# Kernel tuning notes

Hardware: AMD Instinct MI355X
Metric: run time of the kernel (lower is better)

## Reference

```python
import jax, jax.numpy as jnp
import numpy as np
from jax import lax

B, C, T = 4, 512, 2304
H = 16
D = C // H          # 32 head dim
WIN = 19            # window_size
WOV = WIN // 2      # window_overlap = 9
W = 2 * WOV + 1     # band width = 19
EPS = 1e-5          # nn.LayerNorm default eps


def _dwconv(x, w):
    # depthwise Conv1d, kernel 3, pad 1, no bias, groups=C. x:[B,C,T], w:[C,1,3]
    return lax.conv_general_dilated(x, w, (1,), ((1, 1),),
                                    dimension_numbers=('NCH', 'OIH', 'NCH'),
                                    feature_group_count=C)


def _ln_c(x, g, b):
    # LayerNorm over channel dim of [B,C,T] (torch: permute->LN(n_embd)->permute)
    m = jnp.mean(x, axis=1, keepdims=True)
    v = jnp.var(x, axis=1, keepdims=True)
    return (x - m) * lax.rsqrt(v + EPS) * g[None, :, None] + b[None, :, None]


def _pw(x, w, b):
    # 1x1 Conv1d: [B,C,T] x [O,C] -> [B,O,T]
    return jnp.einsum('oc,bct->bot', w, x) + b[None, :, None]


def setup_inputs() -> dict:
    key = jax.random.key(0)
    ks = jax.random.split(key, 10)
    s = lambda shape, k, fan: jax.random.normal(k, shape, jnp.float32) * (1.0 / np.sqrt(fan))
    inp = {
        'x': jax.random.normal(ks[0], (B, C, T), jnp.float32),
        'w_qconv': s((C, 1, 3), ks[1], 3),
        'w_kconv': s((C, 1, 3), ks[2], 3),
        'w_vconv': s((C, 1, 3), ks[3], 3),
        'g_q': jnp.ones((C,), jnp.float32), 'b_q': jnp.zeros((C,), jnp.float32),
        'g_k': jnp.ones((C,), jnp.float32), 'b_k': jnp.zeros((C,), jnp.float32),
        'g_v': jnp.ones((C,), jnp.float32), 'b_v': jnp.zeros((C,), jnp.float32),
        'w_query': s((C, C), ks[4], C), 'b_query': jnp.zeros((C,), jnp.float32),
        'w_key': s((C, C), ks[5], C), 'b_key': jnp.zeros((C,), jnp.float32),
        'w_value': s((C, C), ks[6], C), 'b_value': jnp.zeros((C,), jnp.float32),
        'w_proj': s((C, C), ks[7], C), 'b_proj': jnp.zeros((C,), jnp.float32),
    }
    # realistic variable-length padding mask (valid prefix per sequence)
    lengths = jax.random.randint(ks[8], (B,), T // 2, T + 1)
    inp['mask'] = jnp.arange(T)[None, :] < lengths[:, None]  # [B,T] bool
    return inp


def reference(x, mask, w_qconv, w_kconv, w_vconv, g_q, b_q, g_k, b_k, g_v, b_v,
              w_query, b_query, w_key, b_key, w_value, b_value, w_proj, b_proj):
    mf = mask.astype(x.dtype)[:, None, :]  # [B,1,T]
    # depthwise conv QKV (+ mask) -> LayerNorm -> 1x1 projection
    q = _pw(_ln_c(_dwconv(x, w_qconv) * mf, g_q, b_q), w_query, b_query)
    k = _pw(_ln_c(_dwconv(x, w_kconv) * mf, g_k, b_k), w_key, b_key)
    v = _pw(_ln_c(_dwconv(x, w_vconv) * mf, g_v, b_v), w_value, b_value)
    # split heads: [B,C,T] -> [B,H,T,D] (channel layout C = H*D)
    split = lambda t: t.reshape(B, H, D, T).transpose(0, 1, 3, 2)
    q, k, v = split(q), split(k), split(v)
    scale = 1.0 / np.sqrt(D)
    # banded sliding-window attention: key position for (t, j) is t + j - WOV
    idx = jnp.arange(T)[:, None] + jnp.arange(W)[None, :]  # [T,W] indices into padded axis
    pad4 = lambda t: jnp.pad(t, ((0, 0), (0, 0), (WOV, WOV), (0, 0)))
    kg = pad4(k)[:, :, idx, :]  # [B,H,T,W,D]
    vg = pad4(v)[:, :, idx, :]  # [B,H,T,W,D]
    scores = jnp.einsum('bhtd,bhtwd->bhtw', q, kg) * scale  # [B,H,T,W]
    valid = (idx >= WOV) & (idx < T + WOV)  # in-range key positions [T,W]
    keym = jnp.pad(mask, ((0, 0), (WOV, WOV)))[:, idx]  # [B,T,W] kv padding mask
    addm = jnp.where(keym, 0.0, -1e4).astype(x.dtype)[:, None]  # additive -1e4 like torch
    scores = jnp.where(valid[None, None], scores + addm, -jnp.inf)
    probs = jax.nn.softmax(scores, axis=-1)
    probs = jnp.where(mask[:, None, :, None], probs, 0.0)  # zero masked query rows
    out = jnp.einsum('bhtw,bhtwd->bhtd', probs, vg)  # [B,H,T,D]
    out = out.transpose(0, 1, 3, 2).reshape(B, C, T)
    out = _pw(out, w_proj, b_proj) * mf
    return out, mask
```

## Files before the change

### kernel.cpp

```cpp
#include <hip/hip_runtime.h>
#include <hip/hip_bf16.h>
#include <cstdint>
#include <cstddef>

#define TB 4
#define TC 512
#define TT 2304
#define TH 16
#define TD 32
#define TW 19
#define WOVR 9
#define EPSLN 1e-5f
#define SCALE 0.17677669529663687f
#define MTOT (TB * TT)
#define KSZ  512

typedef __attribute__((ext_vector_type(8))) short s16x8;
typedef __attribute__((ext_vector_type(8))) unsigned short u16x8;
typedef __attribute__((ext_vector_type(4))) float f32x4;

__device__ __forceinline__ float bf2f(unsigned short u) {
  union { unsigned int i; float f; } x; x.i = ((unsigned int)u) << 16; return x.f;
}
__device__ __forceinline__ unsigned short f2bf(float f) {
  union { __hip_bfloat16 h; unsigned short u; } c;
  c.h = __float2bfloat16(f);
  return c.u;
}
__device__ __forceinline__ void gload16(const void* g, void* l) {
  __builtin_amdgcn_global_load_lds(
      (const __attribute__((address_space(1))) unsigned int*)g,
      (__attribute__((address_space(3))) unsigned int*)l, 16, 0, 0);
}

__global__ void k_prep(const unsigned char* __restrict__ mraw,
                       const float* __restrict__ wq, const float* __restrict__ wk,
                       const float* __restrict__ wv, const float* __restrict__ wp,
                       unsigned short* __restrict__ Wbf,
                       float* __restrict__ mf, float* __restrict__ out) {
  const int i = blockIdx.x * 256 + threadIdx.x;
  if (i < 4 * TC * TC) {
    const int z = i >> 18, r = i & (TC * TC - 1);
    const float* src = (z == 0) ? wq : (z == 1) ? wk : (z == 2) ? wv : wp;
    Wbf[i] = f2bf(src[r]);
  }
  if (i < TB * TT) {
    const uint32_t w0 = *(const uint32_t*)mraw;
    bool on;
    if (w0 == 1u)                 on = ((const int*)mraw)[i] != 0;
    else if (w0 == 0x01010101u)   on = mraw[i] != 0;
    else                          on = ((const float*)mraw)[i] != 0.0f;
    const float v = on ? 1.0f : 0.0f;
    mf[i] = v;
    out[(size_t)TB * TC * TT + i] = v;
  }
}

__global__ __launch_bounds__(512) void k_conv_ln_t(
    const float* __restrict__ x,
    const float* __restrict__ wq, const float* __restrict__ wk, const float* __restrict__ wv,
    const float* __restrict__ gq, const float* __restrict__ bq,
    const float* __restrict__ gk, const float* __restrict__ bk,
    const float* __restrict__ gv, const float* __restrict__ bv,
    const float* __restrict__ mf, unsigned short* __restrict__ Aall) {
  const int b = blockIdx.y;
  const int t0 = blockIdx.x * 16;
  const int tid = threadIdx.x;
  const int tt = tid & 15, cg = tid >> 4;
  const int tg = t0 + tt;
  const float m = mf[b * TT + tg];
  __shared__ float ps[3][32][16], ps2[3][32][16];
  __shared__ float mean_s[3][16], rstd_s[3][16];

  float s0 = 0.f, s20 = 0.f, s1 = 0.f, s21 = 0.f, s2v = 0.f, s22 = 0.f;
  unsigned int yp0[8], yp1[8], yp2[8];
  #pragma unroll
  for (int i = 0; i < 16; i++) {
    const int c = cg * 16 + i;
    const float* xp = x + ((size_t)(b * TC + c)) * TT + tg;
    const float xm1 = (tg > 0)      ? xp[-1] : 0.f;
    const float x0  = xp[0];
    const float xp1 = (tg < TT - 1) ? xp[1]  : 0.f;
    const float yq = (wq[c*3] * xm1 + wq[c*3+1] * x0 + wq[c*3+2] * xp1) * m;
    const float yk = (wk[c*3] * xm1 + wk[c*3+1] * x0 + wk[c*3+2] * xp1) * m;
    const float yv = (wv[c*3] * xm1 + wv[c*3+1] * x0 + wv[c*3+2] * xp1) * m;
    s0 += yq; s20 += yq * yq;
    s1 += yk; s21 += yk * yk;
    s2v += yv; s22 += yv * yv;
    const unsigned int hq = f2bf(yq), hk = f2bf(yk), hv = f2bf(yv);
    if ((i & 1) == 0) { yp0[i>>1] = hq; yp1[i>>1] = hk; yp2[i>>1] = hv; }
    else { yp0[i>>1] |= hq << 16; yp1[i>>1] |= hk << 16; yp2[i>>1] |= hv << 16; }
  }
  ps[0][cg][tt] = s0; ps2[0][cg][tt] = s20;
  ps[1][cg][tt] = s1; ps2[1][cg][tt] = s21;
  ps[2][cg][tt] = s2v; ps2[2][cg][tt] = s22;
  __syncthreads();
  if (tid < 48) {
    const int z = tid >> 4, tl = tid & 15;
    float su = 0.f, su2 = 0.f;
    #pragma unroll
    for (int g = 0; g < 32; g++) { su += ps[z][g][tl]; su2 += ps2[z][g][tl]; }
    const float mean = su * (1.f / TC);
    const float var  = su2 * (1.f / TC) - mean * mean;
    mean_s[z][tl] = mean;
    rstd_s[z][tl] = rsqrtf(fmaxf(var, 0.f) + EPSLN);
  }
  __syncthreads();

  #pragma unroll
  for (int z = 0; z < 3; z++) {
    const unsigned int* yp = (z == 0) ? yp0 : (z == 1) ? yp1 : yp2;
    const float* gp = (z == 0) ? gq : (z == 1) ? gk : gv;
    const float* bp = (z == 0) ? bq : (z == 1) ? bk : bv;
    const float mean = mean_s[z][tt], rs = rstd_s[z][tt];
    unsigned short tmp[16];
    #pragma unroll
    for (int i = 0; i < 16; i++) {
      const int c = cg * 16 + i;
      const unsigned short hb =
          (unsigned short)((i & 1) ? (yp[i>>1] >> 16) : (yp[i>>1] & 0xffffu));
      tmp[i] = f2bf((bf2f(hb) - mean) * rs * gp[c] + bp[c]);
    }
    unsigned short* oz = Aall + ((size_t)z * MTOT + b * TT + tg) * TC + cg * 16;
    *(u16x8*)(oz)     = *(const u16x8*)(tmp);
    *(u16x8*)(oz + 8) = *(const u16x8*)(tmp + 8);
  }
}

template<int F32OUT>
__global__ __launch_bounds__(256) void k_gemm_mfma(
    const unsigned short* __restrict__ Abase, const unsigned short* __restrict__ Wbase,
    const float* __restrict__ bq, const float* __restrict__ bk, const float* __restrict__ bv,
    unsigned short* __restrict__ obf, float* __restrict__ of32,
    const float* __restrict__ mf) {
  const int nw = gridDim.x;
  int w = blockIdx.x;
  w = (w & 7) * (nw >> 3) + (w >> 3);
  const int z = w / 288;
  const int rem = w - z * 288;
  const int m0 = (rem >> 2) * 128;
  const int n0 = (rem & 3) * 128;

  const unsigned short* A = Abase + (size_t)z * MTOT * KSZ;
  const unsigned short* W = Wbase + (size_t)z * KSZ * KSZ;
  const float* bias = (z == 0) ? bq : (z == 1) ? bk : bv;

  __shared__ __align__(16) unsigned short smem[6 * 4096];
  const int tid = threadIdx.x;
  const int l = tid & 63, l15 = l & 15, l4 = l >> 4;
  const int wid = tid >> 6, wm = wid >> 1, wn = wid & 1;

  const int r0 = tid >> 2;
  const int c0 = (tid & 3) ^ ((r0 >> 1) & 3);
  const int r1 = r0 + 64;
  const int c1 = (tid & 3) ^ ((r1 >> 1) & 3);
  const size_t gaA0 = (size_t)(m0 + r0) * KSZ + c0 * 8;
  const size_t gaA1 = (size_t)(m0 + r1) * KSZ + c1 * 8;
  const size_t gaB0 = (size_t)(n0 + r0) * KSZ + c0 * 8;
  const size_t gaB1 = (size_t)(n0 + r1) * KSZ + c1 * 8;

  int offA[4], offB[4];
  #pragma unroll
  for (int i = 0; i < 4; i++) {
    const int ra = wm * 64 + i * 16 + l15;
    offA[i] = (ra * 4 + (l4 ^ ((ra >> 1) & 3))) * 8;
    const int rb = wn * 64 + i * 16 + l15;
    offB[i] = (rb * 4 + (l4 ^ ((rb >> 1) & 3))) * 8;
  }

  #define STAGE(buf, kk)                                           \
    do {                                                           \
      unsigned short* Ad = smem + (buf) * 4096;                    \
      unsigned short* Bd = smem + 3 * 4096 + (buf) * 4096;         \
      gload16(A + gaA0 + (kk), Ad + tid * 8);                      \
      gload16(A + gaA1 + (kk), Ad + (tid + 256) * 8);              \
      gload16(W + gaB0 + (kk), Bd + tid * 8);                      \
      gload16(W + gaB1 + (kk), Bd + (tid + 256) * 8);              \
    } while (0)

  f32x4 acc[4][4] = {};
  STAGE(0, 0);
  STAGE(1, 32);
  asm volatile("s_waitcnt vmcnt(4)\ns_barrier" ::: "memory");

  #pragma unroll
  for (int t = 0; t < 16; ++t) {
    if (t + 2 < 16) STAGE((t + 2) % 3, (t + 2) * 32);
    const unsigned short* Ac = smem + (t % 3) * 4096;
    const unsigned short* Bc = smem + 3 * 4096 + (t % 3) * 4096;
    s16x8 av[4], bw[4];
    #pragma unroll
    for (int i = 0; i < 4; i++) {
      av[i] = *(const s16x8*)(Ac + offA[i]);
      bw[i] = *(const s16x8*)(Bc + offB[i]);
    }
    #pragma unroll
    for (int mi = 0; mi < 4; mi++)
      #pragma unroll
      for (int nj = 0; nj < 4; nj++)
        acc[mi][nj] = __builtin_amdgcn_mfma_f32_16x16x32_bf16(
            bw[nj], av[mi], acc[mi][nj], 0, 0, 0);
    if (t < 14)
      asm volatile("s_waitcnt vmcnt(4) lgkmcnt(0)\ns_barrier" ::: "memory");
    else if (t == 14)
      asm volatile("s_waitcnt vmcnt(0) lgkmcnt(0)\ns_barrier" ::: "memory");
  }
  #undef STAGE

  if (!F32OUT) {
    unsigned short* O = obf + (size_t)z * MTOT * KSZ;
    #pragma unroll
    for (int nj = 0; nj < 4; nj++) {
      const int ch0 = n0 + wn * 64 + nj * 16 + l4 * 4;
      const float4 bi = *(const float4*)&bias[ch0];
      #pragma unroll
      for (int mi = 0; mi < 4; mi++) {
        const int bt = m0 + wm * 64 + mi * 16 + l15;
        uint2 pk;
        pk.x = (uint32_t)f2bf(acc[mi][nj][0] + bi.x) |
               ((uint32_t)f2bf(acc[mi][nj][1] + bi.y) << 16);
        pk.y = (uint32_t)f2bf(acc[mi][nj][2] + bi.z) |
               ((uint32_t)f2bf(acc[mi][nj][3] + bi.w) << 16);
        *(uint2*)&O[(size_t)bt * KSZ + ch0] = pk;
      }
    }
  } else {
    const int bb = m0 / TT;
    const int tl0 = m0 - bb * TT;
    #pragma unroll
    for (int mi = 0; mi < 4; mi++) {
      const int bt = m0 + wm * 64 + mi * 16 + l15;
      const int tloc = tl0 + wm * 64 + mi * 16 + l15;
      const float mm = mf[bt];
      #pragma unroll
      for (int nj = 0; nj < 4; nj++) {
        const int ch0 = n0 + wn * 64 + nj * 16 + l4 * 4;
        const float4 bi = *(const float4*)&bias[ch0];
        #pragma unroll
        for (int r = 0; r < 4; r++) {
          const float biv = r == 0 ? bi.x : r == 1 ? bi.y : r == 2 ? bi.z : bi.w;
          of32[((size_t)(bb * TC + ch0 + r)) * TT + tloc] =
              (acc[mi][nj][r] + biv) * mm;
        }
      }
    }
  }
}

#define AROWS (128 + 2 * WOVR)
#define ASTR  36
__global__ __launch_bounds__(256) void k_attn_lds(
    const unsigned short* __restrict__ QKV, const float* __restrict__ mf,
    unsigned short* __restrict__ AO) {
  const int t0 = blockIdx.x * 128;
  const int h = blockIdx.y, b = blockIdx.z;
  const int tid = threadIdx.x;
  const int tloc = tid >> 1, half = tid & 1;
  const size_t SZ = (size_t)MTOT * KSZ;
  const unsigned short* Qp = QKV;
  const unsigned short* Kp = QKV + SZ;
  const unsigned short* Vp = QKV + 2 * SZ;
  __shared__ unsigned short Ks[AROWS * ASTR], Vs[AROWS * ASTR];
  __shared__ float mfs[AROWS];

  for (int idx = tid; idx < 2 * AROWS * 4; idx += 256) {
    const int bufv = idx >= AROWS * 4;
    const int ci = idx - bufv * AROWS * 4;
    const int r = ci >> 2, c = ci & 3;
    const int tk = t0 - WOVR + r;
    const int tkc = tk < 0 ? 0 : (tk >= TT ? TT - 1 : tk);
    const unsigned short* src =
        (bufv ? Vp : Kp) + ((size_t)(b * TT + tkc)) * TC + h * TD + c * 8;
    uint4 v = *(const uint4*)src;
    unsigned short* dst = (bufv ? Vs : Ks) + r * ASTR + c * 8;
    uint2 lo; lo.x = v.x; lo.y = v.y;
    uint2 hi; hi.x = v.z; hi.y = v.w;
    *(uint2*)dst = lo; *(uint2*)(dst + 4) = hi;
  }
  if (tid < AROWS) {
    const int tk = t0 - WOVR + tid;
    mfs[tid] = (tk >= 0 && tk < TT) ? (mf[b * TT + tk] != 0.f ? 0.f : -1e4f)
                                    : -1e30f;
  }
  __syncthreads();

  const int t = t0 + tloc;
  const float qm = mf[b * TT + t];
  float q[16];
  {
    const unsigned short* qr = Qp + ((size_t)(b * TT + t)) * TC + h * TD + half * 16;
    #pragma unroll
    for (int c = 0; c < 2; c++) {
      u16x8 v = *(const u16x8*)(qr + c * 8);
      #pragma unroll
      for (int j = 0; j < 8; j++) q[c * 8 + j] = bf2f(v[j]);
    }
  }
  float e[TW];
  float smax = -3.0e38f;
  #pragma unroll
  for (int j = 0; j < TW; j++) {
    const unsigned short* kr = Ks + (tloc + j) * ASTR + half * 16;
    float acc = 0.f;
    #pragma unroll
    for (int c = 0; c < 4; c++) {
      uint2 w = *(const uint2*)(kr + c * 4);
      acc = fmaf(q[c*4+0], bf2f((unsigned short)(w.x & 0xffffu)), acc);
      acc = fmaf(q[c*4+1], bf2f((unsigned short)(w.x >> 16)), acc);
      acc = fmaf(q[c*4+2], bf2f((unsigned short)(w.y & 0xffffu)), acc);
      acc = fmaf(q[c*4+3], bf2f((unsigned short)(w.y >> 16)), acc);
    }
    acc += __shfl_xor(acc, 1, 64);
    const float sv = acc * SCALE + mfs[tloc + j];
    e[j] = sv;
    smax = fmaxf(smax, sv);
  }
  float den = 0.f;
  #pragma unroll
  for (int j = 0; j < TW; j++) { const float ev = __expf(e[j] - smax); e[j] = ev; den += ev; }
  float o[16] = {};
  #pragma unroll
  for (int j = 0; j < TW; j++) {
    const unsigned short* vr = Vs + (tloc + j) * ASTR + half * 16;
    const float p = e[j];
    #pragma unroll
    for (int c = 0; c < 4; c++) {
      uint2 w = *(const uint2*)(vr + c * 4);
      o[c*4+0] = fmaf(p, bf2f((unsigned short)(w.x & 0xffffu)), o[c*4+0]);
      o[c*4+1] = fmaf(p, bf2f((unsigned short)(w.x >> 16)), o[c*4+1]);
      o[c*4+2] = fmaf(p, bf2f((unsigned short)(w.y & 0xffffu)), o[c*4+2]);
      o[c*4+3] = fmaf(p, bf2f((unsigned short)(w.y >> 16)), o[c*4+3]);
    }
  }
  const float sc = qm / den;
  unsigned short tmp[16];
  #pragma unroll
  for (int i = 0; i < 16; i++) tmp[i] = f2bf(o[i] * sc);
  unsigned short* op = AO + ((size_t)(b * TT + t)) * TC + h * TD + half * 16;
  *(u16x8*)(op)     = *(const u16x8*)(tmp);
  *(u16x8*)(op + 8) = *(const u16x8*)(tmp + 8);
}

extern "C" void kernel_launch(void* const* d_in, const int* in_sizes, int n_in,
                              void* d_out, int out_size, void* d_ws, size_t ws_size,
                              hipStream_t stream) {
  const float* x       = (const float*)d_in[0];
  const float* w_qconv = (const float*)d_in[1];
  const float* w_kconv = (const float*)d_in[2];
  const float* w_vconv = (const float*)d_in[3];
  const float* g_q = (const float*)d_in[4];
  const float* b_q = (const float*)d_in[5];
  const float* g_k = (const float*)d_in[6];
  const float* b_k = (const float*)d_in[7];
  const float* g_v = (const float*)d_in[8];
  const float* b_v = (const float*)d_in[9];
  const float* w_query = (const float*)d_in[10];
  const float* b_query = (const float*)d_in[11];
  const float* w_key   = (const float*)d_in[12];
  const float* b_key   = (const float*)d_in[13];
  const float* w_value = (const float*)d_in[14];
  const float* b_value = (const float*)d_in[15];
  const float* w_proj  = (const float*)d_in[16];
  const float* b_proj  = (const float*)d_in[17];
  const unsigned char* mraw = (const unsigned char*)d_in[18];
  float* out = (float*)d_out;

  uint8_t* w8 = (uint8_t*)d_ws;
  float* mf            = (float*)w8;
  unsigned short* Wbf  = (unsigned short*)(w8 + (1ull << 20));
  unsigned short* Aall = (unsigned short*)(w8 + (4ull << 20));
  unsigned short* QKV  = (unsigned short*)(w8 + (34ull << 20));
  unsigned short* AO   = (unsigned short*)(w8 + (63ull << 20));

  k_prep<<<dim3((4 * TC * TC + 255) / 256), dim3(256), 0, stream>>>(
      mraw, w_query, w_key, w_value, w_proj, Wbf, mf, out);
  k_conv_ln_t<<<dim3(TT / 16, TB), dim3(512), 0, stream>>>(
      x, w_qconv, w_kconv, w_vconv, g_q, b_q, g_k, b_k, g_v, b_v, mf, Aall);
  k_gemm_mfma<0><<<dim3(864), dim3(256), 0, stream>>>(
      Aall, Wbf, b_query, b_key, b_value, QKV, nullptr, mf);
  k_attn_lds<<<dim3(TT / 128, TH, TB), dim3(256), 0, stream>>>(QKV, mf, AO);
  k_gemm_mfma<1><<<dim3(288), dim3(256), 0, stream>>>(
      AO, Wbf + 3 * TC * TC, b_proj, b_proj, b_proj, nullptr, out, mf);
}
```

Measured before the change: 99.19 us.

## Fuse prep into conv+LN kernel, process two timesteps per thread, raise MFMA priority

Removes the separate k_prep launch by folding the weight bf16 conversion and mask materialization into the conv/LayerNorm kernel, which now reads the raw mask directly. Each thread now handles two adjacent timesteps with a float2 load and gets its neighbor halo via wave shuffles instead of three scalar loads, halving the block count. It also pads the shared partial-sum arrays and adds s_setprio around the MFMA block in the GEMM. The aim is to save a launch and cut redundant global loads, at the cost of more registers per thread and fewer blocks.

After: 98.78 us. About the same (-0.4%).

```diff
diff --git a/kernel.cpp b/kernel.cpp
--- a/kernel.cpp
+++ b/kernel.cpp
@@ -32,28 +32,13 @@
       (const __attribute__((address_space(1))) unsigned int*)g,
       (__attribute__((address_space(3))) unsigned int*)l, 16, 0, 0);
 }
-
-__global__ void k_prep(const unsigned char* __restrict__ mraw,
-                       const float* __restrict__ wq, const float* __restrict__ wk,
-                       const float* __restrict__ wv, const float* __restrict__ wp,
-                       unsigned short* __restrict__ Wbf,
-                       float* __restrict__ mf, float* __restrict__ out) {
-  const int i = blockIdx.x * 256 + threadIdx.x;
-  if (i < 4 * TC * TC) {
-    const int z = i >> 18, r = i & (TC * TC - 1);
-    const float* src = (z == 0) ? wq : (z == 1) ? wk : (z == 2) ? wv : wp;
-    Wbf[i] = f2bf(src[r]);
-  }
-  if (i < TB * TT) {
-    const uint32_t w0 = *(const uint32_t*)mraw;
-    bool on;
-    if (w0 == 1u)                 on = ((const int*)mraw)[i] != 0;
-    else if (w0 == 0x01010101u)   on = mraw[i] != 0;
-    else                          on = ((const float*)mraw)[i] != 0.0f;
-    const float v = on ? 1.0f : 0.0f;
-    mf[i] = v;
-    out[(size_t)TB * TC * TT + i] = v;
-  }
+__device__ __forceinline__ float mval(const unsigned char* mraw, int idx) {
+  const uint32_t w0 = *(const uint32_t*)mraw;
+  bool on;
+  if (w0 == 1u)                 on = ((const int*)mraw)[idx] != 0;
+  else if (w0 == 0x01010101u)   on = mraw[idx] != 0;
+  else                          on = ((const float*)mraw)[idx] != 0.0f;
+  return on ? 1.0f : 0.0f;
 }
 
 __global__ __launch_bounds__(512) void k_conv_ln_t(
@@ -62,41 +47,82 @@
     const float* __restrict__ gq, const float* __restrict__ bq,
     const float* __restrict__ gk, const float* __restrict__ bk,
     const float* __restrict__ gv, const float* __restrict__ bv,
-    const float* __restrict__ mf, unsigned short* __restrict__ Aall) {
+    const float* __restrict__ wquery, const float* __restrict__ wkey,
+    const float* __restrict__ wvalue, const float* __restrict__ wproj,
+    const unsigned char* __restrict__ mraw,
+    unsigned short* __restrict__ Wbf, float* __restrict__ mf,
+    float* __restrict__ outtail, unsigned short* __restrict__ Aall) {
   const int b = blockIdx.y;
-  const int t0 = blockIdx.x * 16;
+  const int t0 = blockIdx.x * 32;
   const int tid = threadIdx.x;
   const int tt = tid & 15, cg = tid >> 4;
-  const int tg = t0 + tt;
-  const float m = mf[b * TT + tg];
-  __shared__ float ps[3][32][16], ps2[3][32][16];
-  __shared__ float mean_s[3][16], rstd_s[3][16];
-
-  float s0 = 0.f, s20 = 0.f, s1 = 0.f, s21 = 0.f, s2v = 0.f, s22 = 0.f;
-  unsigned int yp0[8], yp1[8], yp2[8];
+  const int l = tid & 63;
+
+  {
+    const int gtid = (b * 72 + blockIdx.x) * 512 + tid;
+    #pragma unroll
+    for (int rep = 0; rep < 8; rep++) {
+      const int j = gtid + rep * 147456;
+      if (j < 4 * TC * TC) {
+        const int zz = j >> 18, r = j & (TC * TC - 1);
+        const float* src = (zz == 0) ? wquery : (zz == 1) ? wkey
+                          : (zz == 2) ? wvalue : wproj;
+        Wbf[j] = f2bf(src[r]);
+      }
+    }
+    if (gtid < TB * TT) {
+      const float v = mval(mraw, gtid);
+      mf[gtid] = v;
+      outtail[(size_t)TB * TC * TT + gtid] = v;
+    }
+  }
+
+  const int ta = t0 + 2 * tt;
+  const float ma = mval(mraw, b * TT + ta);
+  const float mb = mval(mraw, b * TT + ta + 1);
+
+  __shared__ float ps[3][32][33], ps2[3][32][33];
+  __shared__ float mean_s[3][32], rstd_s[3][32];
+
+  float s[3][2] = {}, s2[3][2] = {};
+  unsigned int yp[3][2][8];
+
+  const int srcm = (l & 48) | ((tt + 15) & 15);
+  const int srcp = (l & 48) | ((tt + 1) & 15);
+
   #pragma unroll
   for (int i = 0; i < 16; i++) {
     const int c = cg * 16 + i;
-    const float* xp = x + ((size_t)(b * TC + c)) * TT + tg;
-    const float xm1 = (tg > 0)      ? xp[-1] : 0.f;
-    const float x0  = xp[0];
-    const float xp1 = (tg < TT - 1) ? xp[1]  : 0.f;
-    const float yq = (wq[c*3] * xm1 + wq[c*3+1] * x0 + wq[c*3+2] * xp1) * m;
-    const float yk = (wk[c*3] * xm1 + wk[c*3+1] * x0 + wk[c*3+2] * xp1) * m;
-    const float yv = (wv[c*3] * xm1 + wv[c*3+1] * x0 + wv[c*3+2] * xp1) * m;
-    s0 += yq; s20 += yq * yq;
-    s1 += yk; s21 += yk * yk;
-    s2v += yv; s22 += yv * yv;
-    const unsigned int hq = f2bf(yq), hk = f2bf(yk), hv = f2bf(yv);
-    if ((i & 1) == 0) { yp0[i>>1] = hq; yp1[i>>1] = hk; yp2[i>>1] = hv; }
-    else { yp0[i>>1] |= hq << 16; yp1[i>>1] |= hk << 16; yp2[i>>1] |= hv << 16; }
-  }
-  ps[0][cg][tt] = s0; ps2[0][cg][tt] = s20;
-  ps[1][cg][tt] = s1; ps2[1][cg][tt] = s21;
-  ps[2][cg][tt] = s2v; ps2[2][cg][tt] = s22;
+    const float* xc = x + ((size_t)(b * TC + c)) * TT;
+    const float2 v = *(const float2*)(xc + ta);
+    float lb = 0.f, rb = 0.f;
+    if (tt == 0 && t0 > 0) lb = xc[t0 - 1];
+    if (tt == 15 && t0 + 32 < TT) rb = xc[t0 + 32];
+    const float shm = __shfl(v.y, srcm, 64);
+    const float shp = __shfl(v.x, srcp, 64);
+    const float xm1 = tt ? shm : lb;
+    const float xp2 = (tt == 15) ? rb : shp;
+    #pragma unroll
+    for (int z = 0; z < 3; z++) {
+      const float* wc = (z == 0) ? wq : (z == 1) ? wk : wv;
+      const float w0 = wc[c * 3], w1 = wc[c * 3 + 1], w2 = wc[c * 3 + 2];
+      const float ya = (w0 * xm1 + w1 * v.x + w2 * v.y) * ma;
+      const float yb = (w0 * v.x + w1 * v.y + w2 * xp2) * mb;
+      s[z][0] += ya; s2[z][0] += ya * ya;
+      s[z][1] += yb; s2[z][1] += yb * yb;
+      const unsigned int ha = f2bf(ya), hb = f2bf(yb);
+      if ((i & 1) == 0) { yp[z][0][i >> 1] = ha; yp[z][1][i >> 1] = hb; }
+      else { yp[z][0][i >> 1] |= ha << 16; yp[z][1][i >> 1] |= hb << 16; }
+    }
+  }
+  #pragma unroll
+  for (int z = 0; z < 3; z++) {
+    ps[z][cg][2 * tt]      = s[z][0]; ps2[z][cg][2 * tt]      = s2[z][0];
+    ps[z][cg][2 * tt + 1]  = s[z][1]; ps2[z][cg][2 * tt + 1]  = s2[z][1];
+  }
   __syncthreads();
-  if (tid < 48) {
-    const int z = tid >> 4, tl = tid & 15;
+  if (tid < 96) {
+    const int z = tid >> 5, tl = tid & 31;
     float su = 0.f, su2 = 0.f;
     #pragma unroll
     for (int g = 0; g < 32; g++) { su += ps[z][g][tl]; su2 += ps2[z][g][tl]; }
@@ -109,21 +135,24 @@
 
   #pragma unroll
   for (int z = 0; z < 3; z++) {
-    const unsigned int* yp = (z == 0) ? yp0 : (z == 1) ? yp1 : yp2;
     const float* gp = (z == 0) ? gq : (z == 1) ? gk : gv;
     const float* bp = (z == 0) ? bq : (z == 1) ? bk : bv;
-    const float mean = mean_s[z][tt], rs = rstd_s[z][tt];
-    unsigned short tmp[16];
-    #pragma unroll
-    for (int i = 0; i < 16; i++) {
-      const int c = cg * 16 + i;
-      const unsigned short hb =
-          (unsigned short)((i & 1) ? (yp[i>>1] >> 16) : (yp[i>>1] & 0xffffu));
-      tmp[i] = f2bf((bf2f(hb) - mean) * rs * gp[c] + bp[c]);
-    }
-    unsigned short* oz = Aall + ((size_t)z * MTOT + b * TT + tg) * TC + cg * 16;
-    *(u16x8*)(oz)     = *(const u16x8*)(tmp);
-    *(u16x8*)(oz + 8) = *(const u16x8*)(tmp + 8);
+    #pragma unroll
+    for (int h = 0; h < 2; h++) {
+      const int t = ta + h;
+      const float mean = mean_s[z][2 * tt + h], rs = rstd_s[z][2 * tt + h];
+      unsigned short tmp[16];
+      #pragma unroll
+      for (int i = 0; i < 16; i++) {
+        const int c = cg * 16 + i;
+        const unsigned short hb = (unsigned short)(
+            (i & 1) ? (yp[z][h][i >> 1] >> 16) : (yp[z][h][i >> 1] & 0xffffu));
+        tmp[i] = f2bf((bf2f(hb) - mean) * rs * gp[c] + bp[c]);
+      }
+      unsigned short* oz = Aall + ((size_t)z * MTOT + b * TT + t) * TC + cg * 16;
+      *(u16x8*)(oz)     = *(const u16x8*)(tmp);
+      *(u16x8*)(oz + 8) = *(const u16x8*)(tmp + 8);
+    }
   }
 }
 
@@ -194,12 +223,14 @@
       av[i] = *(const s16x8*)(Ac + offA[i]);
       bw[i] = *(const s16x8*)(Bc + offB[i]);
     }
+    __builtin_amdgcn_s_setprio(1);
     #pragma unroll
     for (int mi = 0; mi < 4; mi++)
       #pragma unroll
       for (int nj = 0; nj < 4; nj++)
         acc[mi][nj] = __builtin_amdgcn_mfma_f32_16x16x32_bf16(
             bw[nj], av[mi], acc[mi][nj], 0, 0, 0);
+    __builtin_amdgcn_s_setprio(0);
     if (t < 14)
       asm volatile("s_waitcnt vmcnt(4) lgkmcnt(0)\ns_barrier" ::: "memory");
     else if (t == 14)
@@ -372,10 +403,9 @@
   unsigned short* QKV  = (unsigned short*)(w8 + (34ull << 20));
   unsigned short* AO   = (unsigned short*)(w8 + (63ull << 20));
 
-  k_prep<<<dim3((4 * TC * TC + 255) / 256), dim3(256), 0, stream>>>(
-      mraw, w_query, w_key, w_value, w_proj, Wbf, mf, out);
-  k_conv_ln_t<<<dim3(TT / 16, TB), dim3(512), 0, stream>>>(
-      x, w_qconv, w_kconv, w_vconv, g_q, b_q, g_k, b_k, g_v, b_v, mf, Aall);
+  k_conv_ln_t<<<dim3(72, TB), dim3(512), 0, stream>>>(
+      x, w_qconv, w_kconv, w_vconv, g_q, b_q, g_k, b_k, g_v, b_v,
+      w_query, w_key, w_value, w_proj, mraw, Wbf, mf, out, Aall);
   k_gemm_mfma<0><<<dim3(864), dim3(256), 0, stream>>>(
       Aall, Wbf, b_query, b_key, b_value, QKV, nullptr, mf);
   k_attn_lds<<<dim3(TT / 128, TH, TB), dim3(256), 0, stream>>>(QKV, mf, AO);
```
